# Kernel tuning notes

Hardware: AMD Instinct MI355X
Metric: run time of the kernel (lower is better)

The kernel has to match this reference:

```python
import jax, jax.numpy as jnp
import numpy as np

IN_F = 8192
OUT_F = 8192
M = 32  # tokens (small -> memory-bound dequant+GEMV-like)


def setup_inputs() -> dict:
    key = jax.random.key(0)
    k1, k2, k3 = jax.random.split(key, 3)
    x = jax.random.normal(k1, (M, IN_F), dtype=jnp.float32)
    # int8-range quantized weights, stored as int8 like the torch buffer
    weight_quantized = jax.random.randint(k2, (OUT_F, IN_F), -128, 128, dtype=jnp.int32).astype(jnp.int8)
    # positive per-output-channel scales (clamped min 1e-8 in quantize())
    weight_scale = jax.random.uniform(k3, (OUT_F,), dtype=jnp.float32) * 0.02 + 1e-8
    return {"x": x, "weight_quantized": weight_quantized, "weight_scale": weight_scale}


def reference(x, weight_quantized, weight_scale):
    # dequantize: W[o,i] = int8[o,i] * scale[o]  (full fp32 materialization, as in source)
    w = weight_quantized.astype(jnp.float32) * weight_scale[:, None]  # [OUT_F, IN_F]
    # F.linear: x @ W^T
    return jnp.einsum('mi,oi->mo', x, w)
```

## Files before the change

### kernel.cpp

```cpp
#include <hip/hip_runtime.h>
#include <stdint.h>

#define IN_F   8192
#define OUT_F  8192
#define M_TOK  32
#define BN     32
#define BK     128
#define NIT    (IN_F / BK)
#define PF     2
#define LDSS   136

typedef float  f32x4  __attribute__((ext_vector_type(4)));
typedef short  short8 __attribute__((ext_vector_type(8)));

__device__ inline unsigned pk_bf16(float f0, float f1) {
    unsigned u0 = __builtin_bit_cast(unsigned, f0);
    unsigned u1 = __builtin_bit_cast(unsigned, f1);
    return (u0 >> 16) | (u1 & 0xFFFF0000u);
}

__global__ __launch_bounds__(256) void qlin_mfma(
    const float* __restrict__ x, const int* __restrict__ wq,
    const float* __restrict__ scale, float* __restrict__ out) {

    __shared__ ushort ldsA[2][M_TOK][LDSS];
    __shared__ ushort ldsW[2][BN][LDSS];

    const int t  = threadIdx.x;
    const int o0 = blockIdx.x * BN;

    const int r  = t >> 3;
    const int cc = (t & 7) * 16;

    const float* xp = x  + (size_t)r * IN_F + cc;
    const int*   wp = wq + (size_t)(o0 + r) * IN_F + cc;

    float4 abuf[PF][4];
    int4   wbuf[PF][4];

    #pragma unroll
    for (int p = 0; p < PF; ++p) {
        #pragma unroll
        for (int q = 0; q < 4; ++q) {
            abuf[p][q] = *reinterpret_cast<const float4*>(xp + p * BK + 4 * q);
            wbuf[p][q] = *reinterpret_cast<const int4*>(wp + p * BK + 4 * q);
        }
    }

    const int wid  = t >> 6;
    const int lane = t & 63;
    const int mt   = wid & 1;
    const int nt   = wid >> 1;
    const int frow = lane & 15;
    const int fk   = (lane >> 4) * 8;

    f32x4 acc = {0.f, 0.f, 0.f, 0.f};

    for (int base = 0; base < NIT; base += PF) {
        #pragma unroll
        for (int p = 0; p < PF; ++p) {
            const int it  = base + p;
            const int buf = it & 1;

            {
                float4 v0 = abuf[p][0], v1 = abuf[p][1];
                float4 v2 = abuf[p][2], v3 = abuf[p][3];
                uint4 w0, w1;
                w0.x = pk_bf16(v0.x, v0.y); w0.y = pk_bf16(v0.z, v0.w);
                w0.z = pk_bf16(v1.x, v1.y); w0.w = pk_bf16(v1.z, v1.w);
                w1.x = pk_bf16(v2.x, v2.y); w1.y = pk_bf16(v2.z, v2.w);
                w1.z = pk_bf16(v3.x, v3.y); w1.w = pk_bf16(v3.z, v3.w);
                *reinterpret_cast<uint4*>(&ldsA[buf][r][cc])     = w0;
                *reinterpret_cast<uint4*>(&ldsA[buf][r][cc + 8]) = w1;
            }
            {
                int4 a0 = wbuf[p][0], a1 = wbuf[p][1];
                int4 a2 = wbuf[p][2], a3 = wbuf[p][3];
                uint4 w0, w1;
                w0.x = pk_bf16((float)a0.x, (float)a0.y);
                w0.y = pk_bf16((float)a0.z, (float)a0.w);
                w0.z = pk_bf16((float)a1.x, (float)a1.y);
                w0.w = pk_bf16((float)a1.z, (float)a1.w);
                w1.x = pk_bf16((float)a2.x, (float)a2.y);
                w1.y = pk_bf16((float)a2.z, (float)a2.w);
                w1.z = pk_bf16((float)a3.x, (float)a3.y);
                w1.w = pk_bf16((float)a3.z, (float)a3.w);
                *reinterpret_cast<uint4*>(&ldsW[buf][r][cc])     = w0;
                *reinterpret_cast<uint4*>(&ldsW[buf][r][cc + 8]) = w1;
            }

            const int nit = it + PF;
            if (nit < NIT) {
                #pragma unroll
                for (int q = 0; q < 4; ++q) {
                    abuf[p][q] = *reinterpret_cast<const float4*>(xp + nit * BK + 4 * q);
                    wbuf[p][q] = *reinterpret_cast<const int4*>(wp + nit * BK + 4 * q);
                }
            }

            __syncthreads();

            const ushort* aB = &ldsA[buf][mt * 16 + frow][fk];
            const ushort* wB = &ldsW[buf][nt * 16 + frow][fk];
            #pragma unroll
            for (int ks = 0; ks < 4; ++ks) {
                short8 af = *reinterpret_cast<const short8*>(aB + ks * 32);
                short8 bf = *reinterpret_cast<const short8*>(wB + ks * 32);
                acc = __builtin_amdgcn_mfma_f32_16x16x32_bf16(af, bf, acc, 0, 0, 0);
            }
        }
    }

    const int ocol = o0 + nt * 16 + frow;
    const float s  = scale[ocol];
    const int  m0  = mt * 16 + (lane >> 4) * 4;
    #pragma unroll
    for (int rg = 0; rg < 4; ++rg)
        out[(size_t)(m0 + rg) * OUT_F + ocol] = acc[rg] * s;
}

extern "C" void kernel_launch(void* const* d_in, const int* in_sizes, int n_in,
                              void* d_out, int out_size, void* d_ws, size_t ws_size,
                              hipStream_t stream) {
    const float* x  = (const float*)d_in[0];
    const int*   wq = (const int*)d_in[1];
    const float* sc = (const float*)d_in[2];
    float* out = (float*)d_out;

    qlin_mfma<<<OUT_F / BN, 256, 0, stream>>>(x, wq, sc, out);
}
```

Measured before the change: 52.83 us.

## Load MFMA fragments directly from global memory with split-K across waves

```diff
diff --git a/kernel.cpp b/kernel.cpp
--- a/kernel.cpp
+++ b/kernel.cpp
@@ -3,12 +3,10 @@
 
 #define IN_F   8192
 #define OUT_F  8192
-#define M_TOK  32
 #define BN     32
-#define BK     128
-#define NIT    (IN_F / BK)
+#define KG     8
+#define NSTEP  (IN_F / KG / 32)
 #define PF     2
-#define LDSS   136
 
 typedef float  f32x4  __attribute__((ext_vector_type(4)));
 typedef short  short8 __attribute__((ext_vector_type(8)));
@@ -19,104 +17,106 @@
     return (u0 >> 16) | (u1 & 0xFFFF0000u);
 }
 
-__global__ __launch_bounds__(256) void qlin_mfma(
+__device__ inline short8 w_to_bf16(int4 a, int4 b) {
+    uint4 u;
+    u.x = pk_bf16((float)a.x, (float)a.y);
+    u.y = pk_bf16((float)a.z, (float)a.w);
+    u.z = pk_bf16((float)b.x, (float)b.y);
+    u.w = pk_bf16((float)b.z, (float)b.w);
+    return __builtin_bit_cast(short8, u);
+}
+
+__device__ inline short8 x_to_bf16(float4 a, float4 b) {
+    uint4 u;
+    u.x = pk_bf16(a.x, a.y);
+    u.y = pk_bf16(a.z, a.w);
+    u.z = pk_bf16(b.x, b.y);
+    u.w = pk_bf16(b.z, b.w);
+    return __builtin_bit_cast(short8, u);
+}
+
+__global__ __launch_bounds__(1024, 4) void qlin_direct(
     const float* __restrict__ x, const int* __restrict__ wq,
     const float* __restrict__ scale, float* __restrict__ out) {
 
-    __shared__ ushort ldsA[2][M_TOK][LDSS];
-    __shared__ ushort ldsW[2][BN][LDSS];
+    const int t    = threadIdx.x;
+    const int wid  = t >> 6;
+    const int lane = t & 63;
+    const int nt   = wid & 1;
+    const int kg   = wid >> 1;
+    const int o0   = blockIdx.x * BN;
 
-    const int t  = threadIdx.x;
-    const int o0 = blockIdx.x * BN;
+    const int frow = lane & 15;
+    const int fk   = (lane >> 4) * 8;
+    const size_t kbase = (size_t)kg * (IN_F / KG) + fk;
 
-    const int r  = t >> 3;
-    const int cc = (t & 7) * 16;
+    const int*   wp  = wq + (size_t)(o0 + nt * 16 + frow) * IN_F + kbase;
+    const float* xp0 = x  + (size_t)frow        * IN_F + kbase;
+    const float* xp1 = x  + (size_t)(16 + frow) * IN_F + kbase;
 
-    const float* xp = x  + (size_t)r * IN_F + cc;
-    const int*   wp = wq + (size_t)(o0 + r) * IN_F + cc;
-
-    float4 abuf[PF][4];
-    int4   wbuf[PF][4];
+    int4   wa[PF], wb[PF];
+    float4 a0a[PF], a0b[PF], a1a[PF], a1b[PF];
 
     #pragma unroll
     for (int p = 0; p < PF; ++p) {
+        const size_t off = (size_t)p * 32;
+        wa[p]  = *reinterpret_cast<const int4*>(wp + off);
+        wb[p]  = *reinterpret_cast<const int4*>(wp + off + 4);
+        a0a[p] = *reinterpret_cast<const float4*>(xp0 + off);
+        a0b[p] = *reinterpret_cast<const float4*>(xp0 + off + 4);
+        a1a[p] = *reinterpret_cast<const float4*>(xp1 + off);
+        a1b[p] = *reinterpret_cast<const float4*>(xp1 + off + 4);
+    }
+
+    f32x4 acc0 = {0.f, 0.f, 0.f, 0.f};
+    f32x4 acc1 = {0.f, 0.f, 0.f, 0.f};
+
+    for (int s = 0; s < NSTEP; s += PF) {
         #pragma unroll
-        for (int q = 0; q < 4; ++q) {
-            abuf[p][q] = *reinterpret_cast<const float4*>(xp + p * BK + 4 * q);
-            wbuf[p][q] = *reinterpret_cast<const int4*>(wp + p * BK + 4 * q);
+        for (int p = 0; p < PF; ++p) {
+            short8 bw = w_to_bf16(wa[p], wb[p]);
+            short8 f0 = x_to_bf16(a0a[p], a0b[p]);
+            short8 f1 = x_to_bf16(a1a[p], a1b[p]);
+
+            const int ns = s + p + PF;
+            if (ns < NSTEP) {
+                const size_t off = (size_t)ns * 32;
+                wa[p]  = *reinterpret_cast<const int4*>(wp + off);
+                wb[p]  = *reinterpret_cast<const int4*>(wp + off + 4);
+                a0a[p] = *reinterpret_cast<const float4*>(xp0 + off);
+                a0b[p] = *reinterpret_cast<const float4*>(xp0 + off + 4);
+                a1a[p] = *reinterpret_cast<const float4*>(xp1 + off);
+                a1b[p] = *reinterpret_cast<const float4*>(xp1 + off + 4);
+            }
+
+            acc0 = __builtin_amdgcn_mfma_f32_16x16x32_bf16(f0, bw, acc0, 0, 0, 0);
+            acc1 = __builtin_amdgcn_mfma_f32_16x16x32_bf16(f1, bw, acc1, 0, 0, 0);
         }
     }
 
-    const int wid  = t >> 6;
-    const int lane = t & 63;
-    const int mt   = wid & 1;
-    const int nt   = wid >> 1;
-    const int frow = lane & 15;
-    const int fk   = (lane >> 4) * 8;
+    __shared__ f32x4 red[2][KG][64][2];
+    red[nt][kg][lane][0] = acc0;
+    red[nt][kg][lane][1] = acc1;
+    __syncthreads();
 
-    f32x4 acc = {0.f, 0.f, 0.f, 0.f};
-
-    for (int base = 0; base < NIT; base += PF) {
+    if (wid < 2) {
+        const int rnt = wid;
+        f32x4 s0 = red[rnt][0][lane][0];
+        f32x4 s1 = red[rnt][0][lane][1];
         #pragma unroll
-        for (int p = 0; p < PF; ++p) {
-            const int it  = base + p;
-            const int buf = it & 1;
-
-            {
-                float4 v0 = abuf[p][0], v1 = abuf[p][1];
-                float4 v2 = abuf[p][2], v3 = abuf[p][3];
-                uint4 w0, w1;
-                w0.x = pk_bf16(v0.x, v0.y); w0.y = pk_bf16(v0.z, v0.w);
-                w0.z = pk_bf16(v1.x, v1.y); w0.w = pk_bf16(v1.z, v1.w);
-                w1.x = pk_bf16(v2.x, v2.y); w1.y = pk_bf16(v2.z, v2.w);
-                w1.z = pk_bf16(v3.x, v3.y); w1.w = pk_bf16(v3.z, v3.w);
-                *reinterpret_cast<uint4*>(&ldsA[buf][r][cc])     = w0;
-                *reinterpret_cast<uint4*>(&ldsA[buf][r][cc + 8]) = w1;
-            }
-            {
-                int4 a0 = wbuf[p][0], a1 = wbuf[p][1];
-                int4 a2 = wbuf[p][2], a3 = wbuf[p][3];
-                uint4 w0, w1;
-                w0.x = pk_bf16((float)a0.x, (float)a0.y);
-                w0.y = pk_bf16((float)a0.z, (float)a0.w);
-                w0.z = pk_bf16((float)a1.x, (float)a1.y);
-                w0.w = pk_bf16((float)a1.z, (float)a1.w);
-                w1.x = pk_bf16((float)a2.x, (float)a2.y);
-                w1.y = pk_bf16((float)a2.z, (float)a2.w);
-                w1.z = pk_bf16((float)a3.x, (float)a3.y);
-                w1.w = pk_bf16((float)a3.z, (float)a3.w);
-                *reinterpret_cast<uint4*>(&ldsW[buf][r][cc])     = w0;
-                *reinterpret_cast<uint4*>(&ldsW[buf][r][cc + 8]) = w1;
-            }
-
-            const int nit = it + PF;
-            if (nit < NIT) {
-                #pragma unroll
-                for (int q = 0; q < 4; ++q) {
-                    abuf[p][q] = *reinterpret_cast<const float4*>(xp + nit * BK + 4 * q);
-                    wbuf[p][q] = *reinterpret_cast<const int4*>(wp + nit * BK + 4 * q);
-                }
-            }
-
-            __syncthreads();
-
-            const ushort* aB = &ldsA[buf][mt * 16 + frow][fk];
-            const ushort* wB = &ldsW[buf][nt * 16 + frow][fk];
-            #pragma unroll
-            for (int ks = 0; ks < 4; ++ks) {
-                short8 af = *reinterpret_cast<const short8*>(aB + ks * 32);
-                short8 bf = *reinterpret_cast<const short8*>(wB + ks * 32);
-                acc = __builtin_amdgcn_mfma_f32_16x16x32_bf16(af, bf, acc, 0, 0, 0);
-            }
+        for (int g = 1; g < KG; ++g) {
+            s0 += red[rnt][g][lane][0];
+            s1 += red[rnt][g][lane][1];
+        }
+        const int   ocol = o0 + rnt * 16 + frow;
+        const float sc   = scale[ocol];
+        const int   m0   = (lane >> 4) * 4;
+        #pragma unroll
+        for (int rg = 0; rg < 4; ++rg) {
+            out[(size_t)(m0 + rg)      * OUT_F + ocol] = s0[rg] * sc;
+            out[(size_t)(16 + m0 + rg) * OUT_F + ocol] = s1[rg] * sc;
         }
     }
-
-    const int ocol = o0 + nt * 16 + frow;
-    const float s  = scale[ocol];
-    const int  m0  = mt * 16 + (lane >> 4) * 4;
-    #pragma unroll
-    for (int rg = 0; rg < 4; ++rg)
-        out[(size_t)(m0 + rg) * OUT_F + ocol] = acc[rg] * s;
 }
 
 extern "C" void kernel_launch(void* const* d_in, const int* in_sizes, int n_in,
@@ -127,5 +127,5 @@
     const float* sc = (const float*)d_in[2];
     float* out = (float*)d_out;
 
-    qlin_mfma<<<OUT_F / BN, 256, 0, stream>>>(x, wq, sc, out);
+    qlin_direct<<<OUT_F / BN, 1024, 0, stream>>>(x, wq, sc, out);
 }
```

New measurement: 93.18 us. 76.4% more time.
